# Optimization experiments

Measured on AMD Instinct MI355X. Metric: run time of the kernel, lower is better.

Reference implementation:

```python
import jax, jax.numpy as jnp
import numpy as np

N = 25000              # nodes
E = 400000             # edges (avg degree 16)
MUL_S, MUL_V = 64, 32  # irreps_hidden = 64x0e + 32x1o
NB, NH = 8, 64         # num_basis, invariant_neurons
WNUM = 64 + 64 + 32 + 32 + 32  # tp.weight_numel over the 5 uvu paths = 224
AVG_NEI = 16.0
EPS = 1e-5
INV_SQRT3 = 1.0 / np.sqrt(3.0)
INV_SQRT2 = 1.0 / np.sqrt(2.0)


def setup_inputs():
    key = jax.random.key(0)
    ks = jax.random.split(key, 16)
    inp = {}
    inp['node_hiddens'] = jax.random.normal(ks[0], (N, MUL_S + 3 * MUL_V), jnp.float32)
    inp['edge_index'] = jax.random.randint(ks[1], (2, E), 0, N)
    inp['edge_sh'] = jax.random.normal(ks[2], (E, 4), jnp.float32)
    inp['edge_attr'] = jax.random.uniform(ks[3], (E, NB), jnp.float32)
    # linear_1 (per-irrep block mixing)
    inp['W1_0'] = jax.random.normal(ks[4], (MUL_S, MUL_S), jnp.float32)
    inp['W1_1'] = jax.random.normal(ks[5], (MUL_V, MUL_V), jnp.float32)
    # radial MLP [8,64,64,224]
    inp['Wfc1'] = jax.random.normal(ks[6], (NB, NH), jnp.float32)
    inp['Wfc2'] = jax.random.normal(ks[7], (NH, NH), jnp.float32)
    inp['Wfc3'] = jax.random.normal(ks[8], (NH, WNUM), jnp.float32)
    # linear_2: irreps_mid.simplify() = 96x0e + 128x1o -> 64x0e + 32x1o
    inp['W2_0'] = jax.random.normal(ks[9], (96, MUL_S), jnp.float32)
    inp['W2_1'] = jax.random.normal(ks[10], (128, MUL_V), jnp.float32)
    # self-connection linear
    inp['Wsc0'] = jax.random.normal(ks[11], (MUL_S, MUL_S), jnp.float32)
    inp['Wsc1'] = jax.random.normal(ks[12], (MUL_V, MUL_V), jnp.float32)
    # equivariant layernorm affine weights (centering=False -> no bias)
    inp['g0'] = jnp.ones((MUL_S,), jnp.float32)
    inp['g1'] = jnp.ones((MUL_V,), jnp.float32)
    return inp


def _split(x):
    return x[:, :MUL_S], x[:, MUL_S:].reshape(-1, MUL_V, 3)


def _forward(node_hiddens, edge_sh, edge_attr, W1_0, W1_1, Wfc1, Wfc2, Wfc3,
             W2_0, W2_1, Wsc0, Wsc1, g0, g1, edge_src, edge_dst):
    s_in, v_in = _split(node_hiddens)
    # self-connection (e3nn Linear: weight / sqrt(fan_in))
    sc_s = (s_in @ Wsc0) / np.sqrt(MUL_S)
    sc_v = jnp.einsum('nuc,uv->nvc', v_in, Wsc1) / np.sqrt(MUL_V)
    # linear_1
    s = (s_in @ W1_0) / np.sqrt(MUL_S)
    v = jnp.einsum('nuc,uv->nvc', v_in, W1_1) / np.sqrt(MUL_V)
    # radial MLP -> per-edge tensor-product weights [E, 224]
    h = jax.nn.silu(edge_attr @ Wfc1 / np.sqrt(NB))
    h = jax.nn.silu(h @ Wfc2 / np.sqrt(NH))
    w = h @ Wfc3 / np.sqrt(NH)
    w0, w1, w2 = w[:, :64], w[:, 64:128], w[:, 128:160]
    w3, w4 = w[:, 160:192], w[:, 192:224]
    # gather destination node features per edge
    sd = s[edge_dst]            # [E, 64]
    vd = v[edge_dst]            # [E, 32, 3]
    sh0 = edge_sh[:, :1]        # l=0 component
    sh1 = edge_sh[:, 1:4]       # l=1 components
    # uvu tensor-product paths (CG coeffs folded with e3nn component path weights)
    m0 = w0 * sd * sh0                                          # 0e x 0e -> 0e
    m1 = w3 * jnp.sum(vd * sh1[:, None, :], -1) * INV_SQRT3     # 1o x 1o -> 0e
    mv0 = (w1 * sd)[:, :, None] * sh1[:, None, :]               # 0e x 1o -> 1o
    mv1 = w2[:, :, None] * vd * sh0[:, :, None]                 # 1o x 0e -> 1o
    sh1b = jnp.broadcast_to(sh1[:, None, :], vd.shape)
    mv2 = w4[:, :, None] * jnp.cross(vd, sh1b) * INV_SQRT2      # 1o x 1o -> 1o
    mid_s = jnp.concatenate([m0, m1], -1)          # [E, 96]
    mid_v = jnp.concatenate([mv0, mv1, mv2], 1)    # [E, 128, 3]
    # scatter-sum to source nodes, divide by sqrt(avg_num_neighbors)
    ns = jax.ops.segment_sum(mid_s, edge_src, num_segments=N) / np.sqrt(AVG_NEI)
    nv = jax.ops.segment_sum(mid_v, edge_src, num_segments=N) / np.sqrt(AVG_NEI)
    # linear_2 + residual self-connection
    out_s = (ns @ W2_0) / np.sqrt(96) + sc_s
    out_v = jnp.einsum('nuc,uv->nvc', nv, W2_1) / np.sqrt(128) + sc_v
    # equivariant RMS layernorm (centering=False), per irrep block
    rms_s = jnp.sqrt(jnp.mean(out_s ** 2, -1, keepdims=True) + EPS)
    out_s = out_s / rms_s * g0
    rms_v = jnp.sqrt(jnp.mean(jnp.sum(out_v ** 2, -1), -1) + EPS)  # mean over mul of |v|^2
    out_v = out_v / rms_v[:, None, None] * g1[None, :, None]
    return jnp.concatenate([out_s, out_v.reshape(-1, 3 * MUL_V)], -1)


def reference(node_hiddens, edge_index, edge_sh, edge_attr, W1_0, W1_1,
              Wfc1, Wfc2, Wfc3, W2_0, W2_1, Wsc0, Wsc1, g0, g1):
    edge_src = edge_index[0]
    edge_dst = edge_index[1]
    return _forward(node_hiddens, edge_sh, edge_attr, W1_0, W1_1, Wfc1, Wfc2,
                    Wfc3, W2_0, W2_1, Wsc0, Wsc1, g0, g1, edge_src, edge_dst)
```

## Files before the change

kernel.cpp:

```cpp
#include <hip/hip_runtime.h>
#include <hip/hip_fp16.h>

#define N_NODES 25000
#define N_EDGES 400000
#define EPS_F 1e-5f
#define EPB 256

typedef _Float16 f16x8 __attribute__((ext_vector_type(8)));
typedef _Float16 f16x4 __attribute__((ext_vector_type(4)));
typedef float    f32x4 __attribute__((ext_vector_type(4)));

__device__ __forceinline__ float silu_f(float x) {
    return x / (1.0f + __expf(-x));
}

__global__ __launch_bounds__(256) void k_node_pre(
    const float* __restrict__ nh,
    const float* __restrict__ W1_0, const float* __restrict__ W1_1,
    const float* __restrict__ Wsc0, const float* __restrict__ Wsc1,
    float* __restrict__ XS, float* __restrict__ SC)
{
    int n = blockIdx.x * 256 + threadIdx.x;
    if (n >= N_NODES) return;
    const float* row = nh + (size_t)n * 160;
    float* xsrow = XS + (size_t)n * 192;
    float* scrow = SC + (size_t)n * 192;

    float si[64];
#pragma unroll
    for (int m = 0; m < 16; ++m) {
        float4 t = *(const float4*)(row + m * 4);
        si[4*m+0] = t.x; si[4*m+1] = t.y; si[4*m+2] = t.z; si[4*m+3] = t.w;
    }
#pragma unroll 1
    for (int jg = 0; jg < 16; ++jg) {
        float a0=0,a1=0,a2=0,a3=0,b0=0,b1=0,b2=0,b3=0;
#pragma unroll
        for (int k = 0; k < 64; ++k) {
            float wa[4]; *(float4*)wa = *(const float4*)(W1_0 + k*64 + jg*4);
            float wb[4]; *(float4*)wb = *(const float4*)(Wsc0 + k*64 + jg*4);
            float s = si[k];
            a0 += s*wa[0]; a1 += s*wa[1]; a2 += s*wa[2]; a3 += s*wa[3];
            b0 += s*wb[0]; b1 += s*wb[1]; b2 += s*wb[2]; b3 += s*wb[3];
        }
        const float sc8 = 0.125f;
        *(float4*)(xsrow + jg*4) = make_float4(a0*sc8, a1*sc8, a2*sc8, a3*sc8);
        *(float4*)(scrow + jg*4) = make_float4(b0*sc8, b1*sc8, b2*sc8, b3*sc8);
    }

    float vi[96];
#pragma unroll
    for (int m = 0; m < 24; ++m) {
        float4 t = *(const float4*)(row + 64 + m * 4);
        vi[4*m+0] = t.x; vi[4*m+1] = t.y; vi[4*m+2] = t.z; vi[4*m+3] = t.w;
    }
    const float is32 = 0.17677669529663687f;
#pragma unroll 1
    for (int vg = 0; vg < 8; ++vg) {
        float a[4][3], b[4][3];
#pragma unroll
        for (int m = 0; m < 4; ++m) { a[m][0]=a[m][1]=a[m][2]=0.f; b[m][0]=b[m][1]=b[m][2]=0.f; }
#pragma unroll
        for (int u = 0; u < 32; ++u) {
            float wa[4]; *(float4*)wa = *(const float4*)(W1_1 + u*32 + vg*4);
            float wb[4]; *(float4*)wb = *(const float4*)(Wsc1 + u*32 + vg*4);
            float vx = vi[u*3+0], vy = vi[u*3+1], vz = vi[u*3+2];
#pragma unroll
            for (int m = 0; m < 4; ++m) {
                a[m][0] += vx*wa[m]; a[m][1] += vy*wa[m]; a[m][2] += vz*wa[m];
                b[m][0] += vx*wb[m]; b[m][1] += vy*wb[m]; b[m][2] += vz*wb[m];
            }
        }
#pragma unroll
        for (int m = 0; m < 4; ++m) {
            int v = vg*4 + m;
            *(float4*)(xsrow + 64 + v*4) = make_float4(a[m][0]*is32, a[m][1]*is32, a[m][2]*is32, 0.f);
            *(float4*)(scrow + 64 + v*4) = make_float4(b[m][0]*is32, b[m][1]*is32, b[m][2]*is32, 0.f);
        }
    }
}

__global__ __launch_bounds__(256) void k_build_lists(
    const int* __restrict__ ei, int* __restrict__ CNT, int* __restrict__ LIST)
{
    int e = blockIdx.x * 256 + threadIdx.x;
    if (e >= N_EDGES) return;
    int src = ei[e];
    int pos = atomicAdd(&CNT[src], 1);
    if (pos < 64) LIST[src*64 + pos] = e;
}

__global__ __launch_bounds__(256, 2) void k_edge_mlp(
    const float* __restrict__ eat,
    const float* __restrict__ Wfc1, const float* __restrict__ Wfc2,
    const float* __restrict__ Wfc3,
    _Float16* __restrict__ WE)
{
    __shared__ _Float16 sA1[4*64*8];
    __shared__ _Float16 sA2[8*64*8];
    __shared__ _Float16 sA3[28*64*8];
    __shared__ _Float16 avb[64*40];
    __shared__ _Float16 h1b[64*72];
    __shared__ _Float16 h2b[64*72];

    const int tid  = threadIdx.x;
    const int lane = tid & 63, wv = tid >> 6;
    const int q = lane >> 4, col = lane & 15;

    {
        int nt = tid >> 6, L = tid & 63, qq = L >> 4, cc = L & 15;
        _Float16* dst = &sA1[tid*8];
        if (qq == 0) {
#pragma unroll
            for (int j = 0; j < 8; ++j) dst[j] = (_Float16)Wfc1[j*64 + nt*16 + cc];
        } else {
#pragma unroll
            for (int j = 0; j < 8; ++j) dst[j] = (_Float16)0.f;
        }
    }
    for (int t = tid; t < 512; t += 256) {
        int tile = t >> 6, ks = tile >> 2, nt = tile & 3;
        int L = t & 63, qq = L >> 4, cc = L & 15;
        int kb = ks*32 + qq*8;
        _Float16* dst = &sA2[t*8];
#pragma unroll
        for (int j = 0; j < 8; ++j) dst[j] = (_Float16)Wfc2[(kb+j)*64 + nt*16 + cc];
    }
    for (int t = tid; t < 1792; t += 256) {
        int tile = t >> 6, ks = tile / 14, nt = tile - ks*14;
        int L = t & 63, qq = L >> 4, cc = L & 15;
        int kb = ks*32 + qq*8;
        _Float16* dst = &sA3[t*8];
#pragma unroll
        for (int j = 0; j < 8; ++j) dst[j] = (_Float16)Wfc3[(kb+j)*224 + nt*16 + cc];
    }
    for (int idx = tid; idx < 64*12; idx += 256) {
        int e = idx / 12, s = idx - e*12;
        *(unsigned int*)&avb[e*40 + 8 + s*2] = 0u;
    }

    const float IS8 = 0.35355339059327373f;
    size_t base = (size_t)blockIdx.x * EPB;
    const int erow = wv*16 + col;

#pragma unroll 1
    for (int c = 0; c < EPB/64; ++c) {
        size_t cb = base + (size_t)c*64;
        __syncthreads();
        if (tid < 128) {
            int e = tid >> 1, part = tid & 1;
            size_t eg = cb + e; if (eg >= N_EDGES) eg = N_EDGES - 1;
            float4 v = *(const float4*)(eat + eg*8 + part*4);
            f16x4 p; p[0]=(_Float16)v.x; p[1]=(_Float16)v.y; p[2]=(_Float16)v.z; p[3]=(_Float16)v.w;
            *(f16x4*)&avb[e*40 + part*4] = p;
        }
        __syncthreads();

        f16x8 b1 = *(const f16x8*)&avb[erow*40 + q*8];
#pragma unroll
        for (int nt = 0; nt < 4; ++nt) {
            f32x4 acc = {0.f,0.f,0.f,0.f};
            f16x8 a = *(const f16x8*)&sA1[(nt*64 + lane)*8];
            acc = __builtin_amdgcn_mfma_f32_16x16x32_f16(a, b1, acc, 0, 0, 0);
            f16x4 p;
#pragma unroll
            for (int r = 0; r < 4; ++r) p[r] = (_Float16)silu_f(acc[r]*IS8);
            *(f16x4*)&h1b[erow*72 + nt*16 + q*4] = p;
        }
#pragma unroll
        for (int nt = 0; nt < 4; ++nt) {
            f32x4 acc = {0.f,0.f,0.f,0.f};
#pragma unroll
            for (int ks = 0; ks < 2; ++ks) {
                f16x8 a = *(const f16x8*)&sA2[((ks*4+nt)*64 + lane)*8];
                f16x8 b = *(const f16x8*)&h1b[erow*72 + ks*32 + q*8];
                acc = __builtin_amdgcn_mfma_f32_16x16x32_f16(a, b, acc, 0, 0, 0);
            }
            f16x4 p;
#pragma unroll
            for (int r = 0; r < 4; ++r) p[r] = (_Float16)silu_f(acc[r]*0.125f);
            *(f16x4*)&h2b[erow*72 + nt*16 + q*4] = p;
        }
        size_t eg = cb + erow;
        bool wrb = eg < N_EDGES;
#pragma unroll 1
        for (int nt = 0; nt < 14; ++nt) {
            f32x4 acc = {0.f,0.f,0.f,0.f};
#pragma unroll
            for (int ks = 0; ks < 2; ++ks) {
                f16x8 a = *(const f16x8*)&sA3[((ks*14+nt)*64 + lane)*8];
                f16x8 b = *(const f16x8*)&h2b[erow*72 + ks*32 + q*8];
                acc = __builtin_amdgcn_mfma_f32_16x16x32_f16(a, b, acc, 0, 0, 0);
            }
            f16x4 p;
#pragma unroll
            for (int r = 0; r < 4; ++r) p[r] = (_Float16)(acc[r]*0.125f);
            if (wrb) *(f16x4*)&WE[eg*224 + nt*16 + q*4] = p;
        }
    }
}

__global__ __launch_bounds__(256) void k_aggregate(
    const int* __restrict__ ei, const float* __restrict__ esh,
    const _Float16* __restrict__ WE, const float* __restrict__ XS,
    const float* __restrict__ SC, const int* __restrict__ CNT,
    const int* __restrict__ LIST,
    const float* __restrict__ W2_0, const float* __restrict__ W2_1,
    const float* __restrict__ g0, const float* __restrict__ g1,
    float* __restrict__ out)
{
    __shared__ float aS[4][96];
    __shared__ float aV[4][392];
    int tid = threadIdx.x;
    int lane = tid & 63, wave = tid >> 6;
    int n = blockIdx.x*4 + wave;
    bool act = n < N_NODES;
    int u_ = lane & 31;
    bool lo = lane < 32;

    float accM0=0, aV0x=0, aV0y=0, aV0z=0, accM1=0, a12x=0, a12y=0, a12z=0;
    int cnt = 0;
    if (act) { int c = CNT[n]; cnt = c > 64 ? 64 : c; }
    const int* edst = ei + N_EDGES;

    int e_l = 0, dst_l = 0;
    if (act && cnt > 0) {
        int li = lane < cnt ? lane : cnt - 1;
        e_l = LIST[n*64 + li];
        dst_l = edst[e_l];
    }

    float4 sh_c = make_float4(0,0,0,0), vv_c = sh_c;
    unsigned short w0_c=0, w1_c=0, wA_c=0, w3_c=0;
    float sd_c = 0;
    if (cnt > 0) {
        int e = __shfl(e_l, 0), dst = __shfl(dst_l, 0);
        sh_c = *(const float4*)(esh + (size_t)e*4);
        const _Float16* wr = WE + (size_t)e*224;
        w0_c = *(const unsigned short*)(wr + lane);
        w1_c = *(const unsigned short*)(wr + 64 + lane);
        wA_c = *(const unsigned short*)(wr + (lo ? 128 : 192) + u_);
        w3_c = *(const unsigned short*)(wr + 160 + u_);
        const float* xd = XS + (size_t)dst*192;
        sd_c = xd[lane];
        vv_c = *(const float4*)(xd + 64 + u_*4);
    }
    for (int i = 0; i < cnt; ++i) {
        float4 sh = sh_c, vv = vv_c;
        unsigned short w0u = w0_c, w1u = w1_c, wAu = wA_c, w3u = w3_c;
        float sd = sd_c;
        if (i + 1 < cnt) {
            int e = __shfl(e_l, i+1), dst = __shfl(dst_l, i+1);
            sh_c = *(const float4*)(esh + (size_t)e*4);
            const _Float16* wr = WE + (size_t)e*224;
            w0_c = *(const unsigned short*)(wr + lane);
            w1_c = *(const unsigned short*)(wr + 64 + lane);
            wA_c = *(const unsigned short*)(wr + (lo ? 128 : 192) + u_);
            w3_c = *(const unsigned short*)(wr + 160 + u_);
            const float* xd = XS + (size_t)dst*192;
            sd_c = xd[lane];
            vv_c = *(const float4*)(xd + 64 + u_*4);
        }
        float w0 = (float)*(const _Float16*)&w0u;
        float w1 = (float)*(const _Float16*)&w1u;
        float wA = (float)*(const _Float16*)&wAu;
        float w3 = (float)*(const _Float16*)&w3u;
        accM0 += w0*sd*sh.x;
        float t1 = w1*sd;
        aV0x += t1*sh.y; aV0y += t1*sh.z; aV0z += t1*sh.w;
        if (lo) {
            accM1 += w3*(vv.x*sh.y + vv.y*sh.z + vv.z*sh.w);
            a12x += wA*vv.x*sh.x; a12y += wA*vv.y*sh.x; a12z += wA*vv.z*sh.x;
        } else {
            a12x += wA*(vv.y*sh.w - vv.z*sh.z);
            a12y += wA*(vv.z*sh.y - vv.x*sh.w);
            a12z += wA*(vv.x*sh.z - vv.y*sh.y);
        }
    }

    const float SEG = 0.25f;
    const float IS3 = 0.5773502691896258f;
    const float IS2 = 0.7071067811865476f;
    if (act) {
        aS[wave][lane] = accM0 * SEG;
        aV[wave][0*130 + lane] = aV0x * SEG;
        aV[wave][1*130 + lane] = aV0y * SEG;
        aV[wave][2*130 + lane] = aV0z * SEG;
        if (lo) {
            aS[wave][64 + u_] = accM1 * SEG * IS3;
            aV[wave][0*130 + 64 + u_] = a12x * SEG;
            aV[wave][1*130 + 64 + u_] = a12y * SEG;
            aV[wave][2*130 + 64 + u_] = a12z * SEG;
        } else {
            aV[wave][0*130 + 96 + u_] = a12x * SEG * IS2;
            aV[wave][1*130 + 96 + u_] = a12y * SEG * IS2;
            aV[wave][2*130 + 96 + u_] = a12z * SEG * IS2;
        }
    }
    __syncthreads();
    if (!act) return;

    float o0=0,o1=0,o2=0,o3=0;
#pragma unroll 4
    for (int k = 0; k < 96; k += 4) {
        o0 += aS[wave][k+0] * W2_0[(k+0)*64 + lane];
        o1 += aS[wave][k+1] * W2_0[(k+1)*64 + lane];
        o2 += aS[wave][k+2] * W2_0[(k+2)*64 + lane];
        o3 += aS[wave][k+3] * W2_0[(k+3)*64 + lane];
    }
    float os = (o0+o1)+(o2+o3);
    const float IS96 = 0.10206207261596575f;
    os = os*IS96 + SC[(size_t)n*192 + lane];

    int coff = lo ? 0 : 2*130;
    float p0=0,p1=0,q0=0,q1=0;
#pragma unroll 4
    for (int u = 0; u < 128; u += 2) {
        float wv0 = W2_1[(u+0)*32 + u_];
        float wv1 = W2_1[(u+1)*32 + u_];
        p0 += aV[wave][coff + u+0]*wv0;  q0 += aV[wave][130 + u+0]*wv0;
        p1 += aV[wave][coff + u+1]*wv1;  q1 += aV[wave][130 + u+1]*wv1;
    }
    float ov0 = p0+p1, ov1 = q0+q1;
    const float IS128 = 0.08838834764831845f;
    float4 scv = *(const float4*)(SC + (size_t)n*192 + 64 + u_*4);
    float x0 = ov0*IS128 + (lo ? scv.x : scv.z);
    float x1 = ov1*IS128 + scv.y;

    float r = os*os;
#pragma unroll
    for (int off = 32; off > 0; off >>= 1) r += __shfl_xor(r, off);
    float rms_s = sqrtf(r*(1.0f/64.0f) + EPS_F);
    float rv = lo ? (x0*x0 + x1*x1) : (x0*x0);
#pragma unroll
    for (int off = 32; off > 0; off >>= 1) rv += __shfl_xor(rv, off);
    float rms_v = sqrtf(rv*(1.0f/32.0f) + EPS_F);

    float* orow = out + (size_t)n*160;
    orow[lane] = os / rms_s * g0[lane];
    float gv = g1[u_] / rms_v;
    if (lo) {
        orow[64 + u_*3 + 0] = x0 * gv;
        orow[64 + u_*3 + 1] = x1 * gv;
    } else {
        orow[64 + u_*3 + 2] = x0 * gv;
    }
}

extern "C" void kernel_launch(void* const* d_in, const int* in_sizes, int n_in,
                              void* d_out, int out_size, void* d_ws, size_t ws_size,
                              hipStream_t stream)
{
    const float* nh   = (const float*)d_in[0];
    const int*   ei   = (const int*)  d_in[1];
    const float* esh  = (const float*)d_in[2];
    const float* eat  = (const float*)d_in[3];
    const float* W1_0 = (const float*)d_in[4];
    const float* W1_1 = (const float*)d_in[5];
    const float* Wfc1 = (const float*)d_in[6];
    const float* Wfc2 = (const float*)d_in[7];
    const float* Wfc3 = (const float*)d_in[8];
    const float* W2_0 = (const float*)d_in[9];
    const float* W2_1 = (const float*)d_in[10];
    const float* Wsc0 = (const float*)d_in[11];
    const float* Wsc1 = (const float*)d_in[12];
    const float* g0   = (const float*)d_in[13];
    const float* g1   = (const float*)d_in[14];
    float* out = (float*)d_out;

    char* base = (char*)d_ws;
    float*     XS   = (float*)base;
    float*     SC   = XS + (size_t)N_NODES*192;
    _Float16*  WE   = (_Float16*)(SC + (size_t)N_NODES*192);
    int*       CNT  = (int*)(WE + (size_t)N_EDGES*224);
    int*       LIST = CNT + N_NODES;

    hipMemsetAsync(CNT, 0, N_NODES*sizeof(int), stream);
    k_node_pre  <<<(N_NODES+255)/256, 256, 0, stream>>>(nh, W1_0, W1_1, Wsc0, Wsc1, XS, SC);
    k_build_lists<<<(N_EDGES+255)/256, 256, 0, stream>>>(ei, CNT, LIST);
    k_edge_mlp  <<<(N_EDGES+EPB-1)/EPB, 256, 0, stream>>>(eat, Wfc1, Wfc2, Wfc3, WE);
    k_aggregate <<<(N_NODES+3)/4, 256, 0, stream>>>(ei, esh, WE, XS, SC, CNT, LIST,
                                                    W2_0, W2_1, g0, g1, out);
}
```

Before: 406.4 us.

## Fuse edge radial MLP into per-node aggregation kernel and prepack MLP weights

Removes the separate edge-MLP kernel and its global fp16 per-edge weight buffer. Each wave now computes the radial MLP for its node's edge list in 16-edge MFMA tiles, keeping the results in shared memory for the tensor-product accumulation. MLP weights are prepacked once into MFMA layout in global memory and read directly, not staged per block. The node pre-linear kernel is also rewritten to one wave per node using shuffles. This drops the edge-weight write and read but loses MFMA efficiency on partial tiles for low-degree nodes, and makes per-wave work uneven.

```diff
diff --git a/kernel.cpp b/kernel.cpp
--- a/kernel.cpp
+++ b/kernel.cpp
@@ -4,7 +4,6 @@
 #define N_NODES 25000
 #define N_EDGES 400000
 #define EPS_F 1e-5f
-#define EPB 256
 
 typedef _Float16 f16x8 __attribute__((ext_vector_type(8)));
 typedef _Float16 f16x4 __attribute__((ext_vector_type(4)));
@@ -12,6 +11,42 @@
 
 __device__ __forceinline__ float silu_f(float x) {
     return x / (1.0f + __expf(-x));
+}
+
+__global__ __launch_bounds__(256) void k_prepack(
+    const float* __restrict__ Wfc1, const float* __restrict__ Wfc2,
+    const float* __restrict__ Wfc3,
+    _Float16* __restrict__ gA1, _Float16* __restrict__ gA2,
+    _Float16* __restrict__ gA3)
+{
+    int t = blockIdx.x * 256 + threadIdx.x;
+    int L = t & 63, q = L >> 4, cc = L & 15;
+    if (t < 256) {
+        int nt = t >> 6;
+        f16x8 p;
+#pragma unroll
+        for (int j = 0; j < 8; ++j)
+            p[j] = (q == 0) ? (_Float16)Wfc1[j*64 + nt*16 + cc] : (_Float16)0.f;
+        *(f16x8*)&gA1[t*8] = p;
+    } else if (t < 768) {
+        int tt = t - 256;
+        int tile = tt >> 6, ks = tile >> 2, nt = tile & 3;
+        int kb = ks*32 + q*8;
+        f16x8 p;
+#pragma unroll
+        for (int j = 0; j < 8; ++j)
+            p[j] = (_Float16)Wfc2[(kb+j)*64 + nt*16 + cc];
+        *(f16x8*)&gA2[tt*8] = p;
+    } else if (t < 2560) {
+        int tt = t - 768;
+        int tile = tt >> 6, ks = tile / 14, nt = tile - ks*14;
+        int kb = ks*32 + q*8;
+        f16x8 p;
+#pragma unroll
+        for (int j = 0; j < 8; ++j)
+            p[j] = (_Float16)Wfc3[(kb+j)*224 + nt*16 + cc];
+        *(f16x8*)&gA3[tt*8] = p;
+    }
 }
 
 __global__ __launch_bounds__(256) void k_node_pre(
@@ -20,63 +55,51 @@
     const float* __restrict__ Wsc0, const float* __restrict__ Wsc1,
     float* __restrict__ XS, float* __restrict__ SC)
 {
-    int n = blockIdx.x * 256 + threadIdx.x;
+    int lane = threadIdx.x & 63, wv = threadIdx.x >> 6;
+    int n = blockIdx.x*4 + wv;
     if (n >= N_NODES) return;
-    const float* row = nh + (size_t)n * 160;
-    float* xsrow = XS + (size_t)n * 192;
-    float* scrow = SC + (size_t)n * 192;
-
-    float si[64];
-#pragma unroll
-    for (int m = 0; m < 16; ++m) {
-        float4 t = *(const float4*)(row + m * 4);
-        si[4*m+0] = t.x; si[4*m+1] = t.y; si[4*m+2] = t.z; si[4*m+3] = t.w;
-    }
-#pragma unroll 1
-    for (int jg = 0; jg < 16; ++jg) {
-        float a0=0,a1=0,a2=0,a3=0,b0=0,b1=0,b2=0,b3=0;
-#pragma unroll
-        for (int k = 0; k < 64; ++k) {
-            float wa[4]; *(float4*)wa = *(const float4*)(W1_0 + k*64 + jg*4);
-            float wb[4]; *(float4*)wb = *(const float4*)(Wsc0 + k*64 + jg*4);
-            float s = si[k];
-            a0 += s*wa[0]; a1 += s*wa[1]; a2 += s*wa[2]; a3 += s*wa[3];
-            b0 += s*wb[0]; b1 += s*wb[1]; b2 += s*wb[2]; b3 += s*wb[3];
-        }
-        const float sc8 = 0.125f;
-        *(float4*)(xsrow + jg*4) = make_float4(a0*sc8, a1*sc8, a2*sc8, a3*sc8);
-        *(float4*)(scrow + jg*4) = make_float4(b0*sc8, b1*sc8, b2*sc8, b3*sc8);
-    }
-
-    float vi[96];
-#pragma unroll
-    for (int m = 0; m < 24; ++m) {
-        float4 t = *(const float4*)(row + 64 + m * 4);
-        vi[4*m+0] = t.x; vi[4*m+1] = t.y; vi[4*m+2] = t.z; vi[4*m+3] = t.w;
+    int u_ = lane & 31;
+    bool lo = lane < 32;
+    const float* row = nh + n*160;
+
+    float sval = row[lane];
+    float vx = row[64 + u_*3 + 0];
+    float vy = row[64 + u_*3 + 1];
+    float vz = row[64 + u_*3 + 2];
+
+    float as = 0.f, bs = 0.f;
+#pragma unroll 4
+    for (int k = 0; k < 64; ++k) {
+        float sk = __shfl(sval, k);
+        as += sk * W1_0[k*64 + lane];
+        bs += sk * Wsc0[k*64 + lane];
+    }
+    float* xsrow = XS + n*192;
+    float* scrow = SC + n*192;
+    xsrow[lane] = as * 0.125f;
+    scrow[lane] = bs * 0.125f;
+
+    float selv = lo ? vx : vz;
+    int srcbase = lane & 32;
+    float aP=0.f, aQ=0.f, bP=0.f, bQ=0.f;
+#pragma unroll 4
+    for (int u = 0; u < 32; ++u) {
+        float su = __shfl(selv, u | srcbase);
+        float sy = __shfl(vy, u);
+        float wa = W1_1[u*32 + u_];
+        float wb = Wsc1[u*32 + u_];
+        aP += su*wa; aQ += sy*wa;
+        bP += su*wb; bQ += sy*wb;
     }
     const float is32 = 0.17677669529663687f;
-#pragma unroll 1
-    for (int vg = 0; vg < 8; ++vg) {
-        float a[4][3], b[4][3];
-#pragma unroll
-        for (int m = 0; m < 4; ++m) { a[m][0]=a[m][1]=a[m][2]=0.f; b[m][0]=b[m][1]=b[m][2]=0.f; }
-#pragma unroll
-        for (int u = 0; u < 32; ++u) {
-            float wa[4]; *(float4*)wa = *(const float4*)(W1_1 + u*32 + vg*4);
-            float wb[4]; *(float4*)wb = *(const float4*)(Wsc1 + u*32 + vg*4);
-            float vx = vi[u*3+0], vy = vi[u*3+1], vz = vi[u*3+2];
-#pragma unroll
-            for (int m = 0; m < 4; ++m) {
-                a[m][0] += vx*wa[m]; a[m][1] += vy*wa[m]; a[m][2] += vz*wa[m];
-                b[m][0] += vx*wb[m]; b[m][1] += vy*wb[m]; b[m][2] += vz*wb[m];
-            }
-        }
-#pragma unroll
-        for (int m = 0; m < 4; ++m) {
-            int v = vg*4 + m;
-            *(float4*)(xsrow + 64 + v*4) = make_float4(a[m][0]*is32, a[m][1]*is32, a[m][2]*is32, 0.f);
-            *(float4*)(scrow + 64 + v*4) = make_float4(b[m][0]*is32, b[m][1]*is32, b[m][2]*is32, 0.f);
-        }
+    if (lo) {
+        xsrow[64 + u_*4 + 0] = aP * is32;
+        xsrow[64 + u_*4 + 1] = aQ * is32;
+        scrow[64 + u_*4 + 0] = bP * is32;
+        scrow[64 + u_*4 + 1] = bQ * is32;
+    } else {
+        xsrow[64 + u_*4 + 2] = aP * is32;
+        scrow[64 + u_*4 + 2] = bP * is32;
     }
 }
 
@@ -90,77 +113,88 @@
     if (pos < 64) LIST[src*64 + pos] = e;
 }
 
-__global__ __launch_bounds__(256, 2) void k_edge_mlp(
+__global__ __launch_bounds__(256, 2) void k_fused(
+    const int* __restrict__ ei, const float* __restrict__ esh,
     const float* __restrict__ eat,
-    const float* __restrict__ Wfc1, const float* __restrict__ Wfc2,
-    const float* __restrict__ Wfc3,
-    _Float16* __restrict__ WE)
-{
-    __shared__ _Float16 sA1[4*64*8];
-    __shared__ _Float16 sA2[8*64*8];
-    __shared__ _Float16 sA3[28*64*8];
+    const _Float16* __restrict__ gA1, const _Float16* __restrict__ gA2,
+    const _Float16* __restrict__ gA3,
+    const float* __restrict__ XS, const float* __restrict__ SC,
+    const int* __restrict__ CNT, const int* __restrict__ LIST,
+    const float* __restrict__ W2_0, const float* __restrict__ W2_1,
+    const float* __restrict__ g0, const float* __restrict__ g1,
+    float* __restrict__ out)
+{
     __shared__ _Float16 avb[64*40];
     __shared__ _Float16 h1b[64*72];
     __shared__ _Float16 h2b[64*72];
-
-    const int tid  = threadIdx.x;
+    __shared__ _Float16 wt [64*228];
+    __shared__ float aS[4][96];
+    __shared__ float aV[4][392];
+
+    const int tid = threadIdx.x;
     const int lane = tid & 63, wv = tid >> 6;
     const int q = lane >> 4, col = lane & 15;
+    const int u_ = lane & 31;
+    const bool lo = lane < 32;
+    const int erow = wv*16 + col;
+
+    int n = blockIdx.x*4 + wv;
+    if (n >= N_NODES) return;
+
+    int cnt = CNT[n]; cnt = cnt > 64 ? 64 : cnt;
+    const int* edst = ei + N_EDGES;
+
+    int e_l = 0, dst_l = 0;
+    if (cnt > 0) {
+        int li = lane < cnt ? lane : cnt - 1;
+        e_l = LIST[n*64 + li];
+        dst_l = edst[e_l];
+    }
 
     {
-        int nt = tid >> 6, L = tid & 63, qq = L >> 4, cc = L & 15;
-        _Float16* dst = &sA1[tid*8];
-        if (qq == 0) {
-#pragma unroll
-            for (int j = 0; j < 8; ++j) dst[j] = (_Float16)Wfc1[j*64 + nt*16 + cc];
-        } else {
-#pragma unroll
-            for (int j = 0; j < 8; ++j) dst[j] = (_Float16)0.f;
-        }
-    }
-    for (int t = tid; t < 512; t += 256) {
-        int tile = t >> 6, ks = tile >> 2, nt = tile & 3;
-        int L = t & 63, qq = L >> 4, cc = L & 15;
-        int kb = ks*32 + qq*8;
-        _Float16* dst = &sA2[t*8];
-#pragma unroll
-        for (int j = 0; j < 8; ++j) dst[j] = (_Float16)Wfc2[(kb+j)*64 + nt*16 + cc];
-    }
-    for (int t = tid; t < 1792; t += 256) {
-        int tile = t >> 6, ks = tile / 14, nt = tile - ks*14;
-        int L = t & 63, qq = L >> 4, cc = L & 15;
-        int kb = ks*32 + qq*8;
-        _Float16* dst = &sA3[t*8];
-#pragma unroll
-        for (int j = 0; j < 8; ++j) dst[j] = (_Float16)Wfc3[(kb+j)*224 + nt*16 + cc];
-    }
-    for (int idx = tid; idx < 64*12; idx += 256) {
-        int e = idx / 12, s = idx - e*12;
-        *(unsigned int*)&avb[e*40 + 8 + s*2] = 0u;
+        int off0 = lane * 3;
+#pragma unroll
+        for (int z = 0; z < 3; ++z) {
+            int off = off0 + z;
+            int r12 = off / 12, s2 = off - r12*12;
+            *(unsigned int*)&avb[(wv*16 + r12)*40 + 8 + s2*2] = 0u;
+        }
+    }
+
+    float accM0=0, aV0x=0, aV0y=0, aV0z=0, accM1=0, a12x=0, a12y=0, a12z=0;
+
+    float4 sh_c = make_float4(0,0,0,0), vv_c = sh_c;
+    float sd_c = 0;
+    if (cnt > 0) {
+        int e = __shfl(e_l, 0), dst = __shfl(dst_l, 0);
+        sh_c = *(const float4*)(esh + e*4);
+        const float* xd = XS + dst*192;
+        sd_c = xd[lane];
+        vv_c = *(const float4*)(xd + 64 + u_*4);
     }
 
     const float IS8 = 0.35355339059327373f;
-    size_t base = (size_t)blockIdx.x * EPB;
-    const int erow = wv*16 + col;
-
+    int ntiles = (cnt + 15) >> 4;
+    int i = 0;
 #pragma unroll 1
-    for (int c = 0; c < EPB/64; ++c) {
-        size_t cb = base + (size_t)c*64;
-        __syncthreads();
-        if (tid < 128) {
-            int e = tid >> 1, part = tid & 1;
-            size_t eg = cb + e; if (eg >= N_EDGES) eg = N_EDGES - 1;
-            float4 v = *(const float4*)(eat + eg*8 + part*4);
-            f16x4 p; p[0]=(_Float16)v.x; p[1]=(_Float16)v.y; p[2]=(_Float16)v.z; p[3]=(_Float16)v.w;
-            *(f16x4*)&avb[e*40 + part*4] = p;
-        }
-        __syncthreads();
-
+    for (int t = 0; t < ntiles; ++t) {
+        {
+            int idx = t*16 + (lane >> 1);
+            if (idx >= cnt) idx = cnt - 1;
+            int egv = __shfl(e_l, idx);
+            if (lo) {
+                int part = lane & 1;
+                float4 v = *(const float4*)(eat + egv*8 + part*4);
+                f16x4 p; p[0]=(_Float16)v.x; p[1]=(_Float16)v.y;
+                         p[2]=(_Float16)v.z; p[3]=(_Float16)v.w;
+                *(f16x4*)&avb[(wv*16 + (lane>>1))*40 + part*4] = p;
+            }
+        }
         f16x8 b1 = *(const f16x8*)&avb[erow*40 + q*8];
 #pragma unroll
         for (int nt = 0; nt < 4; ++nt) {
             f32x4 acc = {0.f,0.f,0.f,0.f};
-            f16x8 a = *(const f16x8*)&sA1[(nt*64 + lane)*8];
+            f16x8 a = *(const f16x8*)&gA1[(nt*64 + lane)*8];
             acc = __builtin_amdgcn_mfma_f32_16x16x32_f16(a, b1, acc, 0, 0, 0);
             f16x4 p;
 #pragma unroll
@@ -172,7 +206,7 @@
             f32x4 acc = {0.f,0.f,0.f,0.f};
 #pragma unroll
             for (int ks = 0; ks < 2; ++ks) {
-                f16x8 a = *(const f16x8*)&sA2[((ks*4+nt)*64 + lane)*8];
+                f16x8 a = *(const f16x8*)&gA2[((ks*4+nt)*64 + lane)*8];
                 f16x8 b = *(const f16x8*)&h1b[erow*72 + ks*32 + q*8];
                 acc = __builtin_amdgcn_mfma_f32_16x16x32_f16(a, b, acc, 0, 0, 0);
             }
@@ -181,136 +215,80 @@
             for (int r = 0; r < 4; ++r) p[r] = (_Float16)silu_f(acc[r]*0.125f);
             *(f16x4*)&h2b[erow*72 + nt*16 + q*4] = p;
         }
-        size_t eg = cb + erow;
-        bool wrb = eg < N_EDGES;
 #pragma unroll 1
         for (int nt = 0; nt < 14; ++nt) {
             f32x4 acc = {0.f,0.f,0.f,0.f};
 #pragma unroll
             for (int ks = 0; ks < 2; ++ks) {
-                f16x8 a = *(const f16x8*)&sA3[((ks*14+nt)*64 + lane)*8];
+                f16x8 a = *(const f16x8*)&gA3[((ks*14+nt)*64 + lane)*8];
                 f16x8 b = *(const f16x8*)&h2b[erow*72 + ks*32 + q*8];
                 acc = __builtin_amdgcn_mfma_f32_16x16x32_f16(a, b, acc, 0, 0, 0);
             }
             f16x4 p;
 #pragma unroll
             for (int r = 0; r < 4; ++r) p[r] = (_Float16)(acc[r]*0.125f);
-            if (wrb) *(f16x4*)&WE[eg*224 + nt*16 + q*4] = p;
-        }
-    }
-}
-
-__global__ __launch_bounds__(256) void k_aggregate(
-    const int* __restrict__ ei, const float* __restrict__ esh,
-    const _Float16* __restrict__ WE, const float* __restrict__ XS,
-    const float* __restrict__ SC, const int* __restrict__ CNT,
-    const int* __restrict__ LIST,
-    const float* __restrict__ W2_0, const float* __restrict__ W2_1,
-    const float* __restrict__ g0, const float* __restrict__ g1,
-    float* __restrict__ out)
-{
-    __shared__ float aS[4][96];
-    __shared__ float aV[4][392];
-    int tid = threadIdx.x;
-    int lane = tid & 63, wave = tid >> 6;
-    int n = blockIdx.x*4 + wave;
-    bool act = n < N_NODES;
-    int u_ = lane & 31;
-    bool lo = lane < 32;
-
-    float accM0=0, aV0x=0, aV0y=0, aV0z=0, accM1=0, a12x=0, a12y=0, a12z=0;
-    int cnt = 0;
-    if (act) { int c = CNT[n]; cnt = c > 64 ? 64 : c; }
-    const int* edst = ei + N_EDGES;
-
-    int e_l = 0, dst_l = 0;
-    if (act && cnt > 0) {
-        int li = lane < cnt ? lane : cnt - 1;
-        e_l = LIST[n*64 + li];
-        dst_l = edst[e_l];
-    }
-
-    float4 sh_c = make_float4(0,0,0,0), vv_c = sh_c;
-    unsigned short w0_c=0, w1_c=0, wA_c=0, w3_c=0;
-    float sd_c = 0;
-    if (cnt > 0) {
-        int e = __shfl(e_l, 0), dst = __shfl(dst_l, 0);
-        sh_c = *(const float4*)(esh + (size_t)e*4);
-        const _Float16* wr = WE + (size_t)e*224;
-        w0_c = *(const unsigned short*)(wr + lane);
-        w1_c = *(const unsigned short*)(wr + 64 + lane);
-        wA_c = *(const unsigned short*)(wr + (lo ? 128 : 192) + u_);
-        w3_c = *(const unsigned short*)(wr + 160 + u_);
-        const float* xd = XS + (size_t)dst*192;
-        sd_c = xd[lane];
-        vv_c = *(const float4*)(xd + 64 + u_*4);
-    }
-    for (int i = 0; i < cnt; ++i) {
-        float4 sh = sh_c, vv = vv_c;
-        unsigned short w0u = w0_c, w1u = w1_c, wAu = wA_c, w3u = w3_c;
-        float sd = sd_c;
-        if (i + 1 < cnt) {
-            int e = __shfl(e_l, i+1), dst = __shfl(dst_l, i+1);
-            sh_c = *(const float4*)(esh + (size_t)e*4);
-            const _Float16* wr = WE + (size_t)e*224;
-            w0_c = *(const unsigned short*)(wr + lane);
-            w1_c = *(const unsigned short*)(wr + 64 + lane);
-            wA_c = *(const unsigned short*)(wr + (lo ? 128 : 192) + u_);
-            w3_c = *(const unsigned short*)(wr + 160 + u_);
-            const float* xd = XS + (size_t)dst*192;
-            sd_c = xd[lane];
-            vv_c = *(const float4*)(xd + 64 + u_*4);
-        }
-        float w0 = (float)*(const _Float16*)&w0u;
-        float w1 = (float)*(const _Float16*)&w1u;
-        float wA = (float)*(const _Float16*)&wAu;
-        float w3 = (float)*(const _Float16*)&w3u;
-        accM0 += w0*sd*sh.x;
-        float t1 = w1*sd;
-        aV0x += t1*sh.y; aV0y += t1*sh.z; aV0z += t1*sh.w;
-        if (lo) {
-            accM1 += w3*(vv.x*sh.y + vv.y*sh.z + vv.z*sh.w);
-            a12x += wA*vv.x*sh.x; a12y += wA*vv.y*sh.x; a12z += wA*vv.z*sh.x;
-        } else {
-            a12x += wA*(vv.y*sh.w - vv.z*sh.z);
-            a12y += wA*(vv.z*sh.y - vv.x*sh.w);
-            a12z += wA*(vv.x*sh.z - vv.y*sh.y);
+            *(f16x4*)&wt[erow*228 + nt*16 + q*4] = p;
+        }
+        int tc = cnt - t*16; if (tc > 16) tc = 16;
+#pragma unroll 1
+        for (int j = 0; j < tc; ++j, ++i) {
+            float4 sh = sh_c, vv = vv_c;
+            float sd = sd_c;
+            if (i + 1 < cnt) {
+                int e = __shfl(e_l, i+1), dst = __shfl(dst_l, i+1);
+                sh_c = *(const float4*)(esh + e*4);
+                const float* xd = XS + dst*192;
+                sd_c = xd[lane];
+                vv_c = *(const float4*)(xd + 64 + u_*4);
+            }
+            const _Float16* wr = &wt[(wv*16 + j)*228];
+            float w0 = (float)wr[lane];
+            float w1 = (float)wr[64 + lane];
+            float wA = (float)wr[(lo ? 128 : 192) + u_];
+            float w3 = (float)wr[160 + u_];
+            accM0 += w0*sd*sh.x;
+            float t1 = w1*sd;
+            aV0x += t1*sh.y; aV0y += t1*sh.z; aV0z += t1*sh.w;
+            if (lo) {
+                accM1 += w3*(vv.x*sh.y + vv.y*sh.z + vv.z*sh.w);
+                a12x += wA*vv.x*sh.x; a12y += wA*vv.y*sh.x; a12z += wA*vv.z*sh.x;
+            } else {
+                a12x += wA*(vv.y*sh.w - vv.z*sh.z);
+                a12y += wA*(vv.z*sh.y - vv.x*sh.w);
+                a12z += wA*(vv.x*sh.z - vv.y*sh.y);
+            }
         }
     }
 
     const float SEG = 0.25f;
     const float IS3 = 0.5773502691896258f;
     const float IS2 = 0.7071067811865476f;
-    if (act) {
-        aS[wave][lane] = accM0 * SEG;
-        aV[wave][0*130 + lane] = aV0x * SEG;
-        aV[wave][1*130 + lane] = aV0y * SEG;
-        aV[wave][2*130 + lane] = aV0z * SEG;
-        if (lo) {
-            aS[wave][64 + u_] = accM1 * SEG * IS3;
-            aV[wave][0*130 + 64 + u_] = a12x * SEG;
-            aV[wave][1*130 + 64 + u_] = a12y * SEG;
-            aV[wave][2*130 + 64 + u_] = a12z * SEG;
-        } else {
-            aV[wave][0*130 + 96 + u_] = a12x * SEG * IS2;
-            aV[wave][1*130 + 96 + u_] = a12y * SEG * IS2;
-            aV[wave][2*130 + 96 + u_] = a12z * SEG * IS2;
-        }
-    }
-    __syncthreads();
-    if (!act) return;
+    aS[wv][lane] = accM0 * SEG;
+    aV[wv][0*130 + lane] = aV0x * SEG;
+    aV[wv][1*130 + lane] = aV0y * SEG;
+    aV[wv][2*130 + lane] = aV0z * SEG;
+    if (lo) {
+        aS[wv][64 + u_] = accM1 * SEG * IS3;
+        aV[wv][0*130 + 64 + u_] = a12x * SEG;
+        aV[wv][1*130 + 64 + u_] = a12y * SEG;
+        aV[wv][2*130 + 64 + u_] = a12z * SEG;
+    } else {
+        aV[wv][0*130 + 96 + u_] = a12x * SEG * IS2;
+        aV[wv][1*130 + 96 + u_] = a12y * SEG * IS2;
+        aV[wv][2*130 + 96 + u_] = a12z * SEG * IS2;
+    }
 
     float o0=0,o1=0,o2=0,o3=0;
 #pragma unroll 4
     for (int k = 0; k < 96; k += 4) {
-        o0 += aS[wave][k+0] * W2_0[(k+0)*64 + lane];
-        o1 += aS[wave][k+1] * W2_0[(k+1)*64 + lane];
-        o2 += aS[wave][k+2] * W2_0[(k+2)*64 + lane];
-        o3 += aS[wave][k+3] * W2_0[(k+3)*64 + lane];
+        o0 += aS[wv][k+0] * W2_0[(k+0)*64 + lane];
+        o1 += aS[wv][k+1] * W2_0[(k+1)*64 + lane];
+        o2 += aS[wv][k+2] * W2_0[(k+2)*64 + lane];
+        o3 += aS[wv][k+3] * W2_0[(k+3)*64 + lane];
     }
     float os = (o0+o1)+(o2+o3);
     const float IS96 = 0.10206207261596575f;
-    os = os*IS96 + SC[(size_t)n*192 + lane];
+    os = os*IS96 + SC[n*192 + lane];
 
     int coff = lo ? 0 : 2*130;
     float p0=0,p1=0,q0=0,q1=0;
@@ -318,12 +296,12 @@
     for (int u = 0; u < 128; u += 2) {
         float wv0 = W2_1[(u+0)*32 + u_];
         float wv1 = W2_1[(u+1)*32 + u_];
-        p0 += aV[wave][coff + u+0]*wv0;  q0 += aV[wave][130 + u+0]*wv0;
-        p1 += aV[wave][coff + u+1]*wv1;  q1 += aV[wave][130 + u+1]*wv1;
+        p0 += aV[wv][coff + u+0]*wv0;  q0 += aV[wv][130 + u+0]*wv0;
+        p1 += aV[wv][coff + u+1]*wv1;  q1 += aV[wv][130 + u+1]*wv1;
     }
     float ov0 = p0+p1, ov1 = q0+q1;
     const float IS128 = 0.08838834764831845f;
-    float4 scv = *(const float4*)(SC + (size_t)n*192 + 64 + u_*4);
+    float4 scv = *(const float4*)(SC + n*192 + 64 + u_*4);
     float x0 = ov0*IS128 + (lo ? scv.x : scv.z);
     float x1 = ov1*IS128 + scv.y;
 
@@ -336,7 +314,7 @@
     for (int off = 32; off > 0; off >>= 1) rv += __shfl_xor(rv, off);
     float rms_v = sqrtf(rv*(1.0f/32.0f) + EPS_F);
 
-    float* orow = out + (size_t)n*160;
+    float* orow = out + n*160;
     orow[lane] = os / rms_s * g0[lane];
     float gv = g1[u_] / rms_v;
     if (lo) {
@@ -369,16 +347,19 @@
     float* out = (float*)d_out;
 
     char* base = (char*)d_ws;
-    float*     XS   = (float*)base;
-    float*     SC   = XS + (size_t)N_NODES*192;
-    _Float16*  WE   = (_Float16*)(SC + (size_t)N_NODES*192);
-    int*       CNT  = (int*)(WE + (size_t)N_EDGES*224);
-    int*       LIST = CNT + N_NODES;
+    float*    XS   = (float*)base;
+    float*    SC   = XS + (size_t)N_NODES*192;
+    _Float16* gA1  = (_Float16*)(SC + (size_t)N_NODES*192);
+    _Float16* gA2  = gA1 + 2048;
+    _Float16* gA3  = gA2 + 4096;
+    int*      CNT  = (int*)(gA3 + 14336);
+    int*      LIST = CNT + N_NODES;
 
     hipMemsetAsync(CNT, 0, N_NODES*sizeof(int), stream);
-    k_node_pre  <<<(N_NODES+255)/256, 256, 0, stream>>>(nh, W1_0, W1_1, Wsc0, Wsc1, XS, SC);
+    k_prepack   <<<10, 256, 0, stream>>>(Wfc1, Wfc2, Wfc3, gA1, gA2, gA3);
+    k_node_pre  <<<(N_NODES+3)/4, 256, 0, stream>>>(nh, W1_0, W1_1, Wsc0, Wsc1, XS, SC);
     k_build_lists<<<(N_EDGES+255)/256, 256, 0, stream>>>(ei, CNT, LIST);
-    k_edge_mlp  <<<(N_EDGES+EPB-1)/EPB, 256, 0, stream>>>(eat, Wfc1, Wfc2, Wfc3, WE);
-    k_aggregate <<<(N_NODES+3)/4, 256, 0, stream>>>(ei, esh, WE, XS, SC, CNT, LIST,
+    k_fused     <<<(N_NODES+3)/4, 256, 0, stream>>>(ei, esh, eat, gA1, gA2, gA3,
+                                                    XS, SC, CNT, LIST,
                                                     W2_0, W2_1, g0, g1, out);
 }
```

New measurement: 511.2 us. 25.8% more time.
